# Performance work log

Measured on AMD Instinct MI355X. Metric: run time of the kernel, lower is better.

The kernel has to match this reference:

```python
import jax, jax.numpy as jnp
import numpy as np

MASK_THRESHOLD = 0.01
HOTSPOT_PERCENTILE = 90.0
ALPHA = 0.5
EPS = 1e-08


def setup_inputs() -> dict:
    key = jax.random.key(0)
    k1, k2 = jax.random.split(key)
    shape = (8, 1, 128, 128, 128)  # [B, 1, D, H, W]
    pred = jax.random.uniform(k1, shape, dtype=jnp.float32)
    target = jax.random.uniform(k2, shape, dtype=jnp.float32)
    return {"pred": pred, "target": target}


def _masked_quantile(v, q):
    """Quantile (linear interpolation, matching torch.quantile) over entries v > 0.
    Falls back to MASK_THRESHOLD when no valid entries exist."""
    vv = jnp.where(v > 0, v, jnp.nan)
    th = jnp.nanquantile(vv, q)  # ignores nan entries, linear interpolation
    return jnp.where(jnp.isnan(th), jnp.asarray(MASK_THRESHOLD, v.dtype), th)


def _dice_loss_single(p, t, m):
    # p, t, m: [1, D, H, W] for one batch element
    masked_target = (t * m).ravel()
    masked_pred = (p * m).ravel()
    q = HOTSPOT_PERCENTILE / 100.0
    target_threshold = _masked_quantile(masked_target, q)
    pred_threshold = _masked_quantile(masked_pred, q)
    target_hot = (masked_target > target_threshold).astype(p.dtype)
    pred_hot = (masked_pred > pred_threshold).astype(p.dtype)
    intersection = jnp.sum(pred_hot * target_hot)
    union = jnp.sum(pred_hot) + jnp.sum(target_hot) + EPS
    return 1.0 - 2.0 * intersection / union


def reference(pred, target):
    mask = (target > MASK_THRESHOLD).astype(pred.dtype)  # [B,1,D,H,W]
    squared_error = (pred - target) ** 2 * mask
    num_valid = jnp.sum(mask, axis=(1, 2, 3, 4)) + EPS  # [B]
    mse_loss = jnp.sum(squared_error, axis=(1, 2, 3, 4)) / num_valid  # [B]
    dice_loss = jax.vmap(_dice_loss_single)(pred, target, mask)  # [B]
    combined = ALPHA * mse_loss + (1.0 - ALPHA) * dice_loss
    return jnp.mean(combined)  # reduction='mean'
```

## Files before the change

kernel.cpp:

```cpp
#include <hip/hip_runtime.h>

#define NBINS 2048
#define BPB   64
#define TPB   256
#define NB    8
#define UF    4
#define LCAP  512
#define PCAP  8192
#define SCAP  4096

static __device__ __forceinline__ unsigned bucketOf(float v) {
    int b = (int)(v * (float)NBINS);
    if (b < 0) b = 0;
    if (b > NBINS - 1) b = NBINS - 1;
    return (unsigned)b;
}

__global__ __launch_bounds__(TPB) void k_pass1(const float* __restrict__ pred,
                                               const float* __restrict__ targ,
                                               int nvec,
                                               unsigned short* __restrict__ hist16,
                                               double* __restrict__ sse,
                                               unsigned* __restrict__ nvalid)
{
    __shared__ unsigned h[2 * NBINS];
    for (int i = threadIdx.x; i < 2 * NBINS; i += TPB) h[i] = 0u;
    __syncthreads();

    const int b = blockIdx.y;
    const float4* __restrict__ p4 = (const float4*)pred + (size_t)b * nvec;
    const float4* __restrict__ t4 = (const float4*)targ + (size_t)b * nvec;

    float    lsse = 0.f;
    unsigned lnv = 0, lnp = 0;
    const int S = BPB * TPB;

    for (int i0 = blockIdx.x * TPB + threadIdx.x; i0 < nvec; i0 += S * UF) {
        float4 tb[UF], pb[UF];
        if (i0 + (UF - 1) * S < nvec) {
#pragma unroll
            for (int u = 0; u < UF; ++u) { tb[u] = t4[i0 + u * S]; pb[u] = p4[i0 + u * S]; }
#pragma unroll
            for (int u = 0; u < UF; ++u) {
                float tv[4] = {tb[u].x, tb[u].y, tb[u].z, tb[u].w};
                float pv[4] = {pb[u].x, pb[u].y, pb[u].z, pb[u].w};
#pragma unroll
                for (int j = 0; j < 4; ++j) {
                    float tt = tv[j], pp = pv[j];
                    if (tt > 0.01f) {
                        float d = pp - tt;
                        lsse += d * d; lnv++;
                        atomicAdd(&h[bucketOf(tt)], 1u);
                        if (pp > 0.f) { lnp++; atomicAdd(&h[NBINS + bucketOf(pp)], 1u); }
                    }
                }
            }
        } else {
            for (int u = 0; u < UF; ++u) {
                int idx = i0 + u * S;
                if (idx < nvec) {
                    float4 t = t4[idx], p = p4[idx];
                    float tv[4] = {t.x, t.y, t.z, t.w};
                    float pv[4] = {p.x, p.y, p.z, p.w};
                    for (int j = 0; j < 4; ++j) {
                        float tt = tv[j], pp = pv[j];
                        if (tt > 0.01f) {
                            float d = pp - tt;
                            lsse += d * d; lnv++;
                            atomicAdd(&h[bucketOf(tt)], 1u);
                            if (pp > 0.f) { lnp++; atomicAdd(&h[NBINS + bucketOf(pp)], 1u); }
                        }
                    }
                }
            }
        }
    }
    __syncthreads();

    unsigned short* gh = hist16 + ((size_t)b * BPB + blockIdx.x) * (2 * NBINS);
    ushort4* gh4 = (ushort4*)gh;
    for (int i = threadIdx.x; i < (2 * NBINS) / 4; i += TPB) {
        ushort4 v;
        v.x = (unsigned short)h[4 * i + 0];
        v.y = (unsigned short)h[4 * i + 1];
        v.z = (unsigned short)h[4 * i + 2];
        v.w = (unsigned short)h[4 * i + 3];
        gh4[i] = v;
    }

    for (int off = 32; off; off >>= 1) {
        lsse += __shfl_down(lsse, off);
        lnv  += __shfl_down(lnv, off);
        lnp  += __shfl_down(lnp, off);
    }
    if ((threadIdx.x & 63) == 0) {
        atomicAdd(&sse[b], (double)lsse);
        atomicAdd(&nvalid[2 * b + 0], lnv);
        atomicAdd(&nvalid[2 * b + 1], lnp);
    }
}

__global__ __launch_bounds__(256) void k_scan(const unsigned short* __restrict__ hist16,
                                              const unsigned* __restrict__ nvalid,
                                              unsigned* __restrict__ binfo)
{
    const int bt = blockIdx.x;
    const int b = bt >> 1, t = bt & 1;
    const unsigned nv = nvalid[bt];
    unsigned* bi = binfo + bt * 8;

    __shared__ unsigned partial[256];
    __shared__ unsigned sk, sr2;

    if (threadIdx.x == 0) {
        bi[5] = nv;
        if (nv == 0) {
            bi[0] = 0xFFFFFFFFu; bi[1] = 0xFFFFFFFFu;
            bi[2] = 0; bi[3] = 0; bi[4] = __float_as_uint(0.0f);
        } else {
            double pos  = 0.9 * (double)(nv - 1);
            unsigned k  = (unsigned)pos;
            double frac = pos - (double)k;
            bi[3] = k;
            bi[4] = __float_as_uint((float)frac);
            sk = k;
            sr2 = (k + 2 <= nv) ? (k + 2) : (k + 1);
        }
    }
    __syncthreads();
    if (nv == 0) return;

    const unsigned r1 = sk + 1, r2 = sr2;

    const int lo = threadIdx.x * (NBINS / 256);
    unsigned local[NBINS / 256];
#pragma unroll
    for (int j = 0; j < NBINS / 256; ++j) local[j] = 0;
    for (int rep = 0; rep < BPB; ++rep) {
        const ushort4* h4 = (const ushort4*)(hist16 +
            ((size_t)b * BPB + rep) * (2 * NBINS) + (size_t)t * NBINS + lo);
        ushort4 a = h4[0], c = h4[1];
        local[0] += a.x; local[1] += a.y; local[2] += a.z; local[3] += a.w;
        local[4] += c.x; local[5] += c.y; local[6] += c.z; local[7] += c.w;
    }
    unsigned ls = 0;
#pragma unroll
    for (int j = 0; j < NBINS / 256; ++j) ls += local[j];

    partial[threadIdx.x] = ls;
    __syncthreads();
    for (int off = 1; off < 256; off <<= 1) {
        unsigned v = (threadIdx.x >= (unsigned)off) ? partial[threadIdx.x - off] : 0u;
        __syncthreads();
        partial[threadIdx.x] += v;
        __syncthreads();
    }
    unsigned run = partial[threadIdx.x] - ls;

#pragma unroll
    for (int j = 0; j < NBINS / 256; ++j) {
        unsigned c = local[j];
        if (c) {
            if (run < r1 && run + c >= r1) { bi[0] = lo + j; bi[2] = run; }
            if (run < r2 && run + c >= r2) { bi[1] = lo + j; }
        }
        run += c;
    }
}

__global__ __launch_bounds__(TPB) void k_pass2(const float* __restrict__ pred,
                                               const float* __restrict__ targ,
                                               int nvec,
                                               const unsigned* __restrict__ binfo,
                                               unsigned* __restrict__ npairs,
                                               unsigned* __restrict__ naa,
                                               float2* __restrict__ pairs)
{
    __shared__ float2   sbuf[LCAP];
    __shared__ unsigned scnt, sbase;
    if (threadIdx.x == 0) scnt = 0;
    __syncthreads();

    const int b = blockIdx.y;
    const unsigned lo_t = binfo[(2 * b + 0) * 8 + 0], hi_t = binfo[(2 * b + 0) * 8 + 1];
    const unsigned lo_p = binfo[(2 * b + 1) * 8 + 0], hi_p = binfo[(2 * b + 1) * 8 + 1];

    const float4* __restrict__ p4 = (const float4*)pred + (size_t)b * nvec;
    const float4* __restrict__ t4 = (const float4*)targ + (size_t)b * nvec;

    unsigned laa = 0;
    const int S = BPB * TPB;

    for (int i0 = blockIdx.x * TPB + threadIdx.x; i0 < nvec; i0 += S * UF) {
        float4 tb[UF], pb[UF];
        if (i0 + (UF - 1) * S < nvec) {
#pragma unroll
            for (int u = 0; u < UF; ++u) { tb[u] = t4[i0 + u * S]; pb[u] = p4[i0 + u * S]; }
#pragma unroll
            for (int u = 0; u < UF; ++u) {
                float tv[4] = {tb[u].x, tb[u].y, tb[u].z, tb[u].w};
                float pv[4] = {pb[u].x, pb[u].y, pb[u].z, pb[u].w};
#pragma unroll
                for (int j = 0; j < 4; ++j) {
                    float tt = tv[j], pp = pv[j];
                    if (tt > 0.01f) {
                        unsigned at = bucketOf(tt);
                        bool t_in = (at >= lo_t) && (at <= hi_t);
                        bool t_ab = (at > hi_t);
                        bool ppos = (pp > 0.f);
                        unsigned ap = bucketOf(pp);
                        bool p_in = ppos && (ap >= lo_p) && (ap <= hi_p);
                        bool p_ab = ppos && (ap > hi_p);
                        if (t_ab && p_ab) laa++;
                        if (t_in || p_in) {
                            unsigned idx = atomicAdd(&scnt, 1u);
                            if (idx < LCAP) sbuf[idx] = make_float2(tt, pp);
                        }
                    }
                }
            }
        } else {
            for (int u = 0; u < UF; ++u) {
                int idx2 = i0 + u * S;
                if (idx2 < nvec) {
                    float4 t = t4[idx2], p = p4[idx2];
                    float tv[4] = {t.x, t.y, t.z, t.w};
                    float pv[4] = {p.x, p.y, p.z, p.w};
                    for (int j = 0; j < 4; ++j) {
                        float tt = tv[j], pp = pv[j];
                        if (tt > 0.01f) {
                            unsigned at = bucketOf(tt);
                            bool t_in = (at >= lo_t) && (at <= hi_t);
                            bool t_ab = (at > hi_t);
                            bool ppos = (pp > 0.f);
                            unsigned ap = bucketOf(pp);
                            bool p_in = ppos && (ap >= lo_p) && (ap <= hi_p);
                            bool p_ab = ppos && (ap > hi_p);
                            if (t_ab && p_ab) laa++;
                            if (t_in || p_in) {
                                unsigned idx = atomicAdd(&scnt, 1u);
                                if (idx < LCAP) sbuf[idx] = make_float2(tt, pp);
                            }
                        }
                    }
                }
            }
        }
    }
    __syncthreads();
    if (threadIdx.x == 0) {
        unsigned n = scnt < LCAP ? scnt : LCAP;
        sbase = atomicAdd(&npairs[b], n);
        scnt = n;
    }
    __syncthreads();
    for (unsigned i = threadIdx.x; i < scnt; i += TPB) {
        unsigned idx = sbase + i;
        if (idx < PCAP) pairs[(size_t)b * PCAP + idx] = sbuf[i];
    }
    for (int off = 32; off; off >>= 1) laa += __shfl_down(laa, off);
    if ((threadIdx.x & 63) == 0 && laa) atomicAdd(&naa[b], laa);
}

__global__ __launch_bounds__(256) void k_sortsel(const unsigned* __restrict__ binfo,
                                                 const unsigned* __restrict__ npairs,
                                                 const float2* __restrict__ pairs,
                                                 float* __restrict__ thr,
                                                 unsigned* __restrict__ hotc)
{
    __shared__ float s[SCAP];
    __shared__ unsigned scnt, sle;
    __shared__ float sth;

    const int bt = blockIdx.x;
    const int b = bt >> 1, t = bt & 1;
    const unsigned* bi = binfo + bt * 8;
    const unsigned nv = bi[5];
    if (nv == 0) {
        if (threadIdx.x == 0) { thr[bt] = 0.01f; hotc[bt] = 0; }
        return;
    }
    const unsigned lo = bi[0], hi = bi[1];
    if (threadIdx.x == 0) { scnt = 0; sle = 0; }
    __syncthreads();

    unsigned np = npairs[b]; if (np > PCAP) np = PCAP;
    for (unsigned i = threadIdx.x; i < np; i += 256) {
        float2 pr = pairs[(size_t)b * PCAP + i];
        float v = t ? pr.y : pr.x;
        if (v > 0.f) {
            unsigned a = bucketOf(v);
            if (a >= lo && a <= hi) {
                unsigned idx = atomicAdd(&scnt, 1u);
                if (idx < SCAP) s[idx] = v;
            }
        }
    }
    __syncthreads();
    unsigned n = scnt < SCAP ? scnt : SCAP;
    unsigned sn = 1; while (sn < n) sn <<= 1;
    if (sn < 2) sn = 2;
    for (unsigned i = n + threadIdx.x; i < sn; i += 256) s[i] = 3.402823466e+38f;
    __syncthreads();

    for (unsigned ksz = 2; ksz <= sn; ksz <<= 1) {
        for (unsigned j = ksz >> 1; j; j >>= 1) {
            for (unsigned i = threadIdx.x; i < sn; i += 256) {
                unsigned ixj = i ^ j;
                if (ixj > i) {
                    float a = s[i], c = s[ixj];
                    bool up = ((i & ksz) == 0);
                    if ((a > c) == up) { s[i] = c; s[ixj] = a; }
                }
            }
            __syncthreads();
        }
    }

    if (threadIdx.x == 0) {
        unsigned k = bi[3], cb = bi[2];
        float frac = __uint_as_float(bi[4]);
        long idx = (long)k - (long)cb;
        if (idx < 0) idx = 0;
        if (idx >= (long)n) idx = (long)n - 1;
        float v0 = s[idx];
        float v1 = (idx + 1 < (long)n) ? s[idx + 1] : v0;
        sth = v0 + frac * (v1 - v0);
        thr[bt] = sth;
    }
    __syncthreads();
    float th = sth;
    unsigned cle = 0;
    for (unsigned i = threadIdx.x; i < n; i += 256) if (s[i] <= th) cle++;
    for (int off = 32; off; off >>= 1) cle += __shfl_down(cle, off);
    if ((threadIdx.x & 63) == 0 && cle) atomicAdd(&sle, cle);
    __syncthreads();
    if (threadIdx.x == 0) {
        unsigned gle = bi[2] + sle;
        hotc[bt] = nv - gle;
    }
}

__global__ __launch_bounds__(256) void k_final(const double* __restrict__ sse,
                                               const unsigned* __restrict__ nvalid,
                                               const unsigned* __restrict__ naa,
                                               const unsigned* __restrict__ npairs,
                                               const float2* __restrict__ pairs,
                                               const float* __restrict__ thr,
                                               const unsigned* __restrict__ hotc,
                                               float* __restrict__ out)
{
    __shared__ unsigned sI;
    __shared__ double acc;
    if (threadIdx.x == 0) acc = 0.0;
    for (int b = 0; b < NB; ++b) {
        if (threadIdx.x == 0) sI = 0;
        __syncthreads();
        float th_t = thr[2 * b + 0], th_p = thr[2 * b + 1];
        unsigned np = npairs[b]; if (np > PCAP) np = PCAP;
        unsigned c = 0;
        for (unsigned i = threadIdx.x; i < np; i += 256) {
            float2 pr = pairs[(size_t)b * PCAP + i];
            if (pr.x > th_t && pr.y > th_p) c++;
        }
        for (int off = 32; off; off >>= 1) c += __shfl_down(c, off);
        if ((threadIdx.x & 63) == 0 && c) atomicAdd(&sI, c);
        __syncthreads();
        if (threadIdx.x == 0) {
            double nv  = (double)nvalid[2 * b + 0];
            double mse = sse[b] / (nv + 1e-8);
            double T = (double)hotc[2 * b + 0];
            double P = (double)hotc[2 * b + 1];
            double I = (double)(naa[b] + sI);
            double dice = 1.0 - 2.0 * I / (P + T + 1e-8);
            acc += 0.5 * mse + 0.5 * dice;
        }
        __syncthreads();
    }
    if (threadIdx.x == 0) out[0] = (float)(acc / (double)NB);
}

extern "C" void kernel_launch(void* const* d_in, const int* in_sizes, int n_in,
                              void* d_out, int out_size, void* d_ws, size_t ws_size,
                              hipStream_t stream) {
    const float* pred = (const float*)d_in[0];
    const float* targ = (const float*)d_in[1];
    float* out = (float*)d_out;

    const int total = in_sizes[0];
    const int N     = total / NB;
    const int nvec  = N / 4;

    char* ws = (char*)d_ws;
    unsigned short* hist16 = (unsigned short*)(ws + 0);
    double*   sse    = (double*)  (ws + 4194304);
    unsigned* nvalid = (unsigned*)(ws + 4194368);
    unsigned* naa    = (unsigned*)(ws + 4194432);
    unsigned* npairs = (unsigned*)(ws + 4194496);
    unsigned* binfo  = (unsigned*)(ws + 4194560);
    float*    thr    = (float*)   (ws + 4195072);
    unsigned* hotc   = (unsigned*)(ws + 4195136);
    float2*   pairs  = (float2*)  (ws + 4195200);
    (void)ws_size; (void)n_in; (void)out_size;

    hipMemsetAsync(ws + 4194304, 0, 256, stream);

    dim3 gs(BPB, NB);
    k_pass1  <<<gs, TPB, 0, stream>>>(pred, targ, nvec, hist16, sse, nvalid);
    k_scan   <<<2 * NB, 256, 0, stream>>>(hist16, nvalid, binfo);
    k_pass2  <<<gs, TPB, 0, stream>>>(pred, targ, nvec, binfo, npairs, naa, pairs);
    k_sortsel<<<2 * NB, 256, 0, stream>>>(binfo, npairs, pairs, thr, hotc);
    k_final  <<<1, 256, 0, stream>>>(sse, nvalid, naa, npairs, pairs, thr, hotc, out);
}
```

Before: 219.4 us.

## Halve histogram bins, double blocks, software-pipeline streaming loads, split final kernel

Halves the histogram bin count and doubles the blocks per batch so pass1 and pass2 run on a larger grid with less shared memory per block, and adds an occupancy hint to launch bounds. The unrolled 4-way loads are replaced by a double-buffered register prefetch loop that loads the next pair of float4s while the current ones are processed. The final reduction is split into a per-batch resolve kernel launched in parallel plus a tiny final kernel. In exchange there are more candidates per bin, which can enlarge the ambiguous-pair set and risks overflowing the LCAP/PCAP buffers, and one extra kernel launch is added.

```diff
diff --git a/kernel.cpp b/kernel.cpp
--- a/kernel.cpp
+++ b/kernel.cpp
@@ -1,27 +1,24 @@
 #include <hip/hip_runtime.h>
 
-#define NBINS 2048
-#define BPB   64
+#define NBINS 1024
+#define BPB   128
 #define TPB   256
 #define NB    8
-#define UF    4
 #define LCAP  512
 #define PCAP  8192
 #define SCAP  4096
 
 static __device__ __forceinline__ unsigned bucketOf(float v) {
-    int b = (int)(v * (float)NBINS);
-    if (b < 0) b = 0;
-    if (b > NBINS - 1) b = NBINS - 1;
-    return (unsigned)b;
-}
-
-__global__ __launch_bounds__(TPB) void k_pass1(const float* __restrict__ pred,
-                                               const float* __restrict__ targ,
-                                               int nvec,
-                                               unsigned short* __restrict__ hist16,
-                                               double* __restrict__ sse,
-                                               unsigned* __restrict__ nvalid)
+    unsigned b = (unsigned)(v * (float)NBINS);
+    return b > (NBINS - 1) ? (NBINS - 1) : b;
+}
+
+__global__ __launch_bounds__(TPB, 4) void k_pass1(const float* __restrict__ pred,
+                                                  const float* __restrict__ targ,
+                                                  int nvec,
+                                                  unsigned short* __restrict__ hist16,
+                                                  double* __restrict__ sse,
+                                                  unsigned* __restrict__ nvalid)
 {
     __shared__ unsigned h[2 * NBINS];
     for (int i = threadIdx.x; i < 2 * NBINS; i += TPB) h[i] = 0u;
@@ -35,57 +32,54 @@
     unsigned lnv = 0, lnp = 0;
     const int S = BPB * TPB;
 
-    for (int i0 = blockIdx.x * TPB + threadIdx.x; i0 < nvec; i0 += S * UF) {
-        float4 tb[UF], pb[UF];
-        if (i0 + (UF - 1) * S < nvec) {
-#pragma unroll
-            for (int u = 0; u < UF; ++u) { tb[u] = t4[i0 + u * S]; pb[u] = p4[i0 + u * S]; }
-#pragma unroll
-            for (int u = 0; u < UF; ++u) {
-                float tv[4] = {tb[u].x, tb[u].y, tb[u].z, tb[u].w};
-                float pv[4] = {pb[u].x, pb[u].y, pb[u].z, pb[u].w};
-#pragma unroll
-                for (int j = 0; j < 4; ++j) {
-                    float tt = tv[j], pp = pv[j];
-                    if (tt > 0.01f) {
-                        float d = pp - tt;
-                        lsse += d * d; lnv++;
-                        atomicAdd(&h[bucketOf(tt)], 1u);
-                        if (pp > 0.f) { lnp++; atomicAdd(&h[NBINS + bucketOf(pp)], 1u); }
-                    }
-                }
-            }
-        } else {
-            for (int u = 0; u < UF; ++u) {
-                int idx = i0 + u * S;
-                if (idx < nvec) {
-                    float4 t = t4[idx], p = p4[idx];
-                    float tv[4] = {t.x, t.y, t.z, t.w};
-                    float pv[4] = {p.x, p.y, p.z, p.w};
-                    for (int j = 0; j < 4; ++j) {
-                        float tt = tv[j], pp = pv[j];
-                        if (tt > 0.01f) {
-                            float d = pp - tt;
-                            lsse += d * d; lnv++;
-                            atomicAdd(&h[bucketOf(tt)], 1u);
-                            if (pp > 0.f) { lnp++; atomicAdd(&h[NBINS + bucketOf(pp)], 1u); }
-                        }
-                    }
-                }
-            }
-        }
-    }
+#define P1_PROC(tq, pq)                                          \
+    {                                                            \
+        float tv[4] = {tq.x, tq.y, tq.z, tq.w};                  \
+        float pv[4] = {pq.x, pq.y, pq.z, pq.w};                  \
+        _Pragma("unroll")                                        \
+        for (int j = 0; j < 4; ++j) {                            \
+            float tt = tv[j], pp = pv[j];                        \
+            if (tt > 0.01f) {                                    \
+                float d = pp - tt;                               \
+                lsse += d * d; lnv++;                            \
+                atomicAdd(&h[bucketOf(tt)], 1u);                 \
+                if (pp > 0.f) {                                  \
+                    lnp++;                                       \
+                    atomicAdd(&h[NBINS + bucketOf(pp)], 1u);     \
+                }                                                \
+            }                                                    \
+        }                                                        \
+    }
+
+    int i = blockIdx.x * TPB + threadIdx.x;
+    float4 cT0, cP0, cT1, cP1;
+    cT0 = cP0 = cT1 = cP1 = make_float4(0.f, 0.f, 0.f, 0.f);
+    if (i < nvec) {
+        cT0 = t4[i]; cP0 = p4[i];
+        if (i + S < nvec) { cT1 = t4[i + S]; cP1 = p4[i + S]; }
+    }
+    while (i < nvec) {
+        const int nx = i + 2 * S;
+        float4 nT0 = cT0, nP0 = cP0, nT1 = cT1, nP1 = cP1;
+        if (nx < nvec)     { nT0 = t4[nx];     nP0 = p4[nx]; }
+        if (nx + S < nvec) { nT1 = t4[nx + S]; nP1 = p4[nx + S]; }
+        P1_PROC(cT0, cP0);
+        if (i + S < nvec) P1_PROC(cT1, cP1);
+        cT0 = nT0; cP0 = nP0; cT1 = nT1; cP1 = nP1;
+        i = nx;
+    }
+#undef P1_PROC
     __syncthreads();
 
     unsigned short* gh = hist16 + ((size_t)b * BPB + blockIdx.x) * (2 * NBINS);
     ushort4* gh4 = (ushort4*)gh;
-    for (int i = threadIdx.x; i < (2 * NBINS) / 4; i += TPB) {
+    for (int k = threadIdx.x; k < (2 * NBINS) / 4; k += TPB) {
         ushort4 v;
-        v.x = (unsigned short)h[4 * i + 0];
-        v.y = (unsigned short)h[4 * i + 1];
-        v.z = (unsigned short)h[4 * i + 2];
-        v.w = (unsigned short)h[4 * i + 3];
-        gh4[i] = v;
+        v.x = (unsigned short)h[4 * k + 0];
+        v.y = (unsigned short)h[4 * k + 1];
+        v.z = (unsigned short)h[4 * k + 2];
+        v.w = (unsigned short)h[4 * k + 3];
+        gh4[k] = v;
     }
 
     for (int off = 32; off; off >>= 1) {
@@ -139,9 +133,8 @@
     for (int rep = 0; rep < BPB; ++rep) {
         const ushort4* h4 = (const ushort4*)(hist16 +
             ((size_t)b * BPB + rep) * (2 * NBINS) + (size_t)t * NBINS + lo);
-        ushort4 a = h4[0], c = h4[1];
+        ushort4 a = h4[0];
         local[0] += a.x; local[1] += a.y; local[2] += a.z; local[3] += a.w;
-        local[4] += c.x; local[5] += c.y; local[6] += c.z; local[7] += c.w;
     }
     unsigned ls = 0;
 #pragma unroll
@@ -168,13 +161,13 @@
     }
 }
 
-__global__ __launch_bounds__(TPB) void k_pass2(const float* __restrict__ pred,
-                                               const float* __restrict__ targ,
-                                               int nvec,
-                                               const unsigned* __restrict__ binfo,
-                                               unsigned* __restrict__ npairs,
-                                               unsigned* __restrict__ naa,
-                                               float2* __restrict__ pairs)
+__global__ __launch_bounds__(TPB, 4) void k_pass2(const float* __restrict__ pred,
+                                                  const float* __restrict__ targ,
+                                                  int nvec,
+                                                  const unsigned* __restrict__ binfo,
+                                                  unsigned* __restrict__ npairs,
+                                                  unsigned* __restrict__ naa,
+                                                  float2* __restrict__ pairs)
 {
     __shared__ float2   sbuf[LCAP];
     __shared__ unsigned scnt, sbase;
@@ -191,62 +184,48 @@
     unsigned laa = 0;
     const int S = BPB * TPB;
 
-    for (int i0 = blockIdx.x * TPB + threadIdx.x; i0 < nvec; i0 += S * UF) {
-        float4 tb[UF], pb[UF];
-        if (i0 + (UF - 1) * S < nvec) {
-#pragma unroll
-            for (int u = 0; u < UF; ++u) { tb[u] = t4[i0 + u * S]; pb[u] = p4[i0 + u * S]; }
-#pragma unroll
-            for (int u = 0; u < UF; ++u) {
-                float tv[4] = {tb[u].x, tb[u].y, tb[u].z, tb[u].w};
-                float pv[4] = {pb[u].x, pb[u].y, pb[u].z, pb[u].w};
-#pragma unroll
-                for (int j = 0; j < 4; ++j) {
-                    float tt = tv[j], pp = pv[j];
-                    if (tt > 0.01f) {
-                        unsigned at = bucketOf(tt);
-                        bool t_in = (at >= lo_t) && (at <= hi_t);
-                        bool t_ab = (at > hi_t);
-                        bool ppos = (pp > 0.f);
-                        unsigned ap = bucketOf(pp);
-                        bool p_in = ppos && (ap >= lo_p) && (ap <= hi_p);
-                        bool p_ab = ppos && (ap > hi_p);
-                        if (t_ab && p_ab) laa++;
-                        if (t_in || p_in) {
-                            unsigned idx = atomicAdd(&scnt, 1u);
-                            if (idx < LCAP) sbuf[idx] = make_float2(tt, pp);
-                        }
-                    }
-                }
-            }
-        } else {
-            for (int u = 0; u < UF; ++u) {
-                int idx2 = i0 + u * S;
-                if (idx2 < nvec) {
-                    float4 t = t4[idx2], p = p4[idx2];
-                    float tv[4] = {t.x, t.y, t.z, t.w};
-                    float pv[4] = {p.x, p.y, p.z, p.w};
-                    for (int j = 0; j < 4; ++j) {
-                        float tt = tv[j], pp = pv[j];
-                        if (tt > 0.01f) {
-                            unsigned at = bucketOf(tt);
-                            bool t_in = (at >= lo_t) && (at <= hi_t);
-                            bool t_ab = (at > hi_t);
-                            bool ppos = (pp > 0.f);
-                            unsigned ap = bucketOf(pp);
-                            bool p_in = ppos && (ap >= lo_p) && (ap <= hi_p);
-                            bool p_ab = ppos && (ap > hi_p);
-                            if (t_ab && p_ab) laa++;
-                            if (t_in || p_in) {
-                                unsigned idx = atomicAdd(&scnt, 1u);
-                                if (idx < LCAP) sbuf[idx] = make_float2(tt, pp);
-                            }
-                        }
-                    }
-                }
-            }
-        }
-    }
+#define P2_PROC(tq, pq)                                                   \
+    {                                                                     \
+        float tv[4] = {tq.x, tq.y, tq.z, tq.w};                           \
+        float pv[4] = {pq.x, pq.y, pq.z, pq.w};                           \
+        _Pragma("unroll")                                                 \
+        for (int j = 0; j < 4; ++j) {                                     \
+            float tt = tv[j], pp = pv[j];                                 \
+            if (tt > 0.01f) {                                             \
+                unsigned at = bucketOf(tt);                               \
+                bool t_in = (at >= lo_t) && (at <= hi_t);                 \
+                bool t_ab = (at > hi_t);                                  \
+                bool ppos = (pp > 0.f);                                   \
+                unsigned ap = bucketOf(pp);                               \
+                bool p_in = ppos && (ap >= lo_p) && (ap <= hi_p);         \
+                bool p_ab = ppos && (ap > hi_p);                          \
+                if (t_ab && p_ab) laa++;                                  \
+                if (t_in || p_in) {                                       \
+                    unsigned idx = atomicAdd(&scnt, 1u);                  \
+                    if (idx < LCAP) sbuf[idx] = make_float2(tt, pp);      \
+                }                                                         \
+            }                                                             \
+        }                                                                 \
+    }
+
+    int i = blockIdx.x * TPB + threadIdx.x;
+    float4 cT0, cP0, cT1, cP1;
+    cT0 = cP0 = cT1 = cP1 = make_float4(0.f, 0.f, 0.f, 0.f);
+    if (i < nvec) {
+        cT0 = t4[i]; cP0 = p4[i];
+        if (i + S < nvec) { cT1 = t4[i + S]; cP1 = p4[i + S]; }
+    }
+    while (i < nvec) {
+        const int nx = i + 2 * S;
+        float4 nT0 = cT0, nP0 = cP0, nT1 = cT1, nP1 = cP1;
+        if (nx < nvec)     { nT0 = t4[nx];     nP0 = p4[nx]; }
+        if (nx + S < nvec) { nT1 = t4[nx + S]; nP1 = p4[nx + S]; }
+        P2_PROC(cT0, cP0);
+        if (i + S < nvec) P2_PROC(cT1, cP1);
+        cT0 = nT0; cP0 = nP0; cT1 = nT1; cP1 = nP1;
+        i = nx;
+    }
+#undef P2_PROC
     __syncthreads();
     if (threadIdx.x == 0) {
         unsigned n = scnt < LCAP ? scnt : LCAP;
@@ -254,9 +233,9 @@
         scnt = n;
     }
     __syncthreads();
-    for (unsigned i = threadIdx.x; i < scnt; i += TPB) {
-        unsigned idx = sbase + i;
-        if (idx < PCAP) pairs[(size_t)b * PCAP + idx] = sbuf[i];
+    for (unsigned k = threadIdx.x; k < scnt; k += TPB) {
+        unsigned idx = sbase + k;
+        if (idx < PCAP) pairs[(size_t)b * PCAP + idx] = sbuf[k];
     }
     for (int off = 32; off; off >>= 1) laa += __shfl_down(laa, off);
     if ((threadIdx.x & 63) == 0 && laa) atomicAdd(&naa[b], laa);
@@ -341,43 +320,48 @@
     }
 }
 
-__global__ __launch_bounds__(256) void k_final(const double* __restrict__ sse,
-                                               const unsigned* __restrict__ nvalid,
-                                               const unsigned* __restrict__ naa,
-                                               const unsigned* __restrict__ npairs,
-                                               const float2* __restrict__ pairs,
-                                               const float* __restrict__ thr,
-                                               const unsigned* __restrict__ hotc,
-                                               float* __restrict__ out)
+__global__ __launch_bounds__(256) void k_resolve(const unsigned* __restrict__ npairs,
+                                                 const float2* __restrict__ pairs,
+                                                 const float* __restrict__ thr,
+                                                 unsigned* __restrict__ iamb)
 {
     __shared__ unsigned sI;
-    __shared__ double acc;
-    if (threadIdx.x == 0) acc = 0.0;
-    for (int b = 0; b < NB; ++b) {
-        if (threadIdx.x == 0) sI = 0;
-        __syncthreads();
-        float th_t = thr[2 * b + 0], th_p = thr[2 * b + 1];
-        unsigned np = npairs[b]; if (np > PCAP) np = PCAP;
-        unsigned c = 0;
-        for (unsigned i = threadIdx.x; i < np; i += 256) {
-            float2 pr = pairs[(size_t)b * PCAP + i];
-            if (pr.x > th_t && pr.y > th_p) c++;
-        }
-        for (int off = 32; off; off >>= 1) c += __shfl_down(c, off);
-        if ((threadIdx.x & 63) == 0 && c) atomicAdd(&sI, c);
-        __syncthreads();
-        if (threadIdx.x == 0) {
+    if (threadIdx.x == 0) sI = 0;
+    __syncthreads();
+    const int b = blockIdx.x;
+    float th_t = thr[2 * b + 0], th_p = thr[2 * b + 1];
+    unsigned np = npairs[b]; if (np > PCAP) np = PCAP;
+    unsigned c = 0;
+    for (unsigned i = threadIdx.x; i < np; i += 256) {
+        float2 pr = pairs[(size_t)b * PCAP + i];
+        if (pr.x > th_t && pr.y > th_p) c++;
+    }
+    for (int off = 32; off; off >>= 1) c += __shfl_down(c, off);
+    if ((threadIdx.x & 63) == 0 && c) atomicAdd(&sI, c);
+    __syncthreads();
+    if (threadIdx.x == 0) iamb[b] = sI;
+}
+
+__global__ void k_final(const double* __restrict__ sse,
+                        const unsigned* __restrict__ nvalid,
+                        const unsigned* __restrict__ naa,
+                        const unsigned* __restrict__ iamb,
+                        const unsigned* __restrict__ hotc,
+                        float* __restrict__ out)
+{
+    if (threadIdx.x == 0 && blockIdx.x == 0) {
+        double acc = 0.0;
+        for (int b = 0; b < NB; ++b) {
             double nv  = (double)nvalid[2 * b + 0];
             double mse = sse[b] / (nv + 1e-8);
             double T = (double)hotc[2 * b + 0];
             double P = (double)hotc[2 * b + 1];
-            double I = (double)(naa[b] + sI);
+            double I = (double)(naa[b] + iamb[b]);
             double dice = 1.0 - 2.0 * I / (P + T + 1e-8);
             acc += 0.5 * mse + 0.5 * dice;
         }
-        __syncthreads();
-    }
-    if (threadIdx.x == 0) out[0] = (float)(acc / (double)NB);
+        out[0] = (float)(acc / (double)NB);
+    }
 }
 
 extern "C" void kernel_launch(void* const* d_in, const int* in_sizes, int n_in,
@@ -400,15 +384,17 @@
     unsigned* binfo  = (unsigned*)(ws + 4194560);
     float*    thr    = (float*)   (ws + 4195072);
     unsigned* hotc   = (unsigned*)(ws + 4195136);
-    float2*   pairs  = (float2*)  (ws + 4195200);
+    unsigned* iamb   = (unsigned*)(ws + 4195200);
+    float2*   pairs  = (float2*)  (ws + 4195264);
     (void)ws_size; (void)n_in; (void)out_size;
 
-    hipMemsetAsync(ws + 4194304, 0, 256, stream);
+    hipMemsetAsync(ws + 4194304, 0, 960, stream);
 
     dim3 gs(BPB, NB);
     k_pass1  <<<gs, TPB, 0, stream>>>(pred, targ, nvec, hist16, sse, nvalid);
     k_scan   <<<2 * NB, 256, 0, stream>>>(hist16, nvalid, binfo);
     k_pass2  <<<gs, TPB, 0, stream>>>(pred, targ, nvec, binfo, npairs, naa, pairs);
     k_sortsel<<<2 * NB, 256, 0, stream>>>(binfo, npairs, pairs, thr, hotc);
-    k_final  <<<1, 256, 0, stream>>>(sse, nvalid, naa, npairs, pairs, thr, hotc, out);
-}
+    k_resolve<<<NB, 256, 0, stream>>>(npairs, pairs, thr, iamb);
+    k_final  <<<1, 64, 0, stream>>>(sse, nvalid, naa, iamb, hotc, out);
+}
```

Result: slower. 343.8 us (+56.7%).
